# Kernel tuning notes

Measured on AMD Instinct MI355X. Metric: run time of the kernel, lower is better.

## Reference

```python
import jax, jax.numpy as jnp
import numpy as np

EMBED, VOCAB, NUM_DIGEST, EXPAND = 128, 50257, 4, 4


def _mueller_hash(k):
    # https://stackoverflow.com/a/12996028 , uint32 wraparound semantics
    k = (k >> np.uint32(16) ^ k) * np.uint32(73244475)
    k = (k >> np.uint32(16) ^ k) * np.uint32(73244475)
    k = k >> np.uint32(16) ^ k
    return k


def setup_inputs() -> dict:
    key = jax.random.key(0)
    k_tok, k_tab, k_w1, k_w2 = jax.random.split(key, 4)
    # bloom ledger hash indices (exact replication of bloom_ledger)
    ids = np.arange(VOCAB, dtype=np.uint32)
    i_list, j_list = [], []
    for _ in range(NUM_DIGEST):
        ids = _mueller_hash(ids)
        i_list.append(ids % VOCAB)
        ids = _mueller_hash(ids)
        j_list.append(ids % VOCAB)
    bloom_i = jnp.asarray(np.concatenate(i_list).astype(np.int32))
    bloom_j = jnp.asarray(np.concatenate(j_list).astype(np.int32))
    hidden = EMBED * EXPAND
    return {
        "tokens": jax.random.randint(k_tok, (8, 4096), 0, VOCAB, dtype=jnp.int32),
        "table": jax.random.normal(k_tab, (VOCAB, EMBED), jnp.float32) / np.sqrt(EMBED),
        "bloom_i": bloom_i,
        "bloom_j": bloom_j,
        "w1": jax.random.normal(k_w1, (EMBED, hidden), jnp.float32) / np.sqrt(EMBED),
        "b1": jnp.zeros((hidden,), jnp.float32),
        "w2": jax.random.normal(k_w2, (hidden, EMBED), jnp.float32) / np.sqrt(hidden),
        "b2": jnp.zeros((EMBED,), jnp.float32),
    }


def reference(tokens, table, bloom_i, bloom_j, w1, b1, w2, b2):
    vocab = table.shape[0]
    num_digest = bloom_i.shape[0] // vocab
    scale = jnp.asarray(1.0 / np.sqrt(num_digest), table.dtype)
    # bloom @ table as a scatter-add: A[i] += scale * table[j]  -> [vocab, embed]
    agg = jnp.zeros_like(table).at[bloom_i].add(scale * table[bloom_j])
    # one_hot(tokens) @ (bloom @ table) == row gather
    x = agg[tokens]                      # [B, S, embed]
    h = jax.nn.gelu(x @ w1 + b1)         # [B, S, hidden]
    return h @ w2 + b2                   # [B, S, embed]
```

## Files before the change

### kernel.cpp

```cpp
#include <hip/hip_runtime.h>
#include <hip/hip_bf16.h>
#include <stdint.h>

#define EMBED  128
#define HIDDEN 512
#define TB     64
#define CAP    32

typedef __attribute__((ext_vector_type(8))) short short8v;
typedef __attribute__((ext_vector_type(4))) float f32x4;

__device__ __forceinline__ ushort f2bf(float f) {
    uint32_t b = __float_as_uint(f);
    uint32_t r = (b + 0x7FFFu + ((b >> 16) & 1u)) >> 16;
    return (ushort)r;
}

__device__ __forceinline__ float gelu_fast(float x) {
    float x2 = x * x;
    float u  = x * fmaf(0.035677408136f, x2, 0.7978845608f);
    float t  = __expf(2.0f * u);
    return x - x * __frcp_rn(t + 1.0f);
}

__global__ __launch_bounds__(256)
void prep_kernel(const float* __restrict__ w1, const float* __restrict__ w2,
                 ushort* __restrict__ W1t, ushort* __restrict__ W2t,
                 int* __restrict__ cnt, int vocab) {
    __shared__ float T[32][33];
    int b = blockIdx.x;
    int t = threadIdx.x;
    if (b < 128) {
        const float* in; ushort* outp; int inCols, outCols, tr, tc;
        if (b < 64) {
            in = w1; outp = W1t; inCols = 512; outCols = 128;
            tr = b >> 4; tc = b & 15;
        } else {
            int b2 = b - 64;
            in = w2; outp = W2t; inCols = 128; outCols = 512;
            tr = b2 >> 2; tc = b2 & 3;
        }
        int r  = t >> 3;
        int c4 = (t & 7) * 4;
        float4 v = *(const float4*)&in[(size_t)(tr * 32 + r) * inCols + tc * 32 + c4];
        T[c4 + 0][r] = v.x; T[c4 + 1][r] = v.y; T[c4 + 2][r] = v.z; T[c4 + 3][r] = v.w;
        __syncthreads();
        ushort o[4];
        #pragma unroll
        for (int i = 0; i < 4; ++i) o[i] = f2bf(T[r][c4 + i]);
        *(ushort4*)&outp[(size_t)(tc * 32 + r) * outCols + tr * 32 + c4] = *(ushort4*)o;
    } else {
        int i = (b - 128) * 256 + t;
        if (i < vocab) cnt[i] = 0;
    }
}

__global__ __launch_bounds__(256)
void bucket_kernel(const int* __restrict__ bi, const int* __restrict__ bj,
                   int* __restrict__ cnt, int* __restrict__ csr, int nk) {
    int k = blockIdx.x * blockDim.x + threadIdx.x;
    if (k >= nk) return;
    int i = bi[k];
    int slot = atomicAdd(&cnt[i], 1);
    if (slot < CAP) csr[(size_t)i * CAP + slot] = bj[k];
}

__global__ __launch_bounds__(512)
void mlp_mfma_kernel(const int*    __restrict__ tokens,
                     const float*  __restrict__ table,
                     const int*    __restrict__ cnt,
                     const int*    __restrict__ csr,
                     const ushort* __restrict__ W1t,
                     const ushort* __restrict__ W2t,
                     const float*  __restrict__ b1,
                     const float*  __restrict__ b2,
                     float*        __restrict__ out) {
    __shared__ ushort Xs[TB * EMBED];
    __shared__ ushort Hs[TB * HIDDEN];

    const int t    = threadIdx.x;
    const int lane = t & 63;
    const int wv   = t >> 6;
    const int base = blockIdx.x * TB;
    const int l15  = lane & 15;
    const int lhi  = lane >> 4;

    {
        int r    = t >> 3;
        int coff = (t & 7) * 16;
        int tok  = tokens[base + r];
        int m    = min(cnt[tok], CAP);
        const int* jrow = csr + (size_t)tok * CAP;
        f32x4 xa0 = {0.f,0.f,0.f,0.f}, xa1 = {0.f,0.f,0.f,0.f};
        f32x4 xa2 = {0.f,0.f,0.f,0.f}, xa3 = {0.f,0.f,0.f,0.f};
        for (int e = 0; e < m; ++e) {
            int j = jrow[e];
            const float* trp = table + (size_t)j * EMBED + coff;
            float4 v0 = *(const float4*)(trp);
            float4 v1 = *(const float4*)(trp + 4);
            float4 v2 = *(const float4*)(trp + 8);
            float4 v3 = *(const float4*)(trp + 12);
            xa0 += (f32x4){v0.x, v0.y, v0.z, v0.w};
            xa1 += (f32x4){v1.x, v1.y, v1.z, v1.w};
            xa2 += (f32x4){v2.x, v2.y, v2.z, v2.w};
            xa3 += (f32x4){v3.x, v3.y, v3.z, v3.w};
        }
        ushort u[16];
        #pragma unroll
        for (int q = 0; q < 4; ++q) {
            u[q]      = f2bf(0.5f * xa0[q]);
            u[4 + q]  = f2bf(0.5f * xa1[q]);
            u[8 + q]  = f2bf(0.5f * xa2[q]);
            u[12 + q] = f2bf(0.5f * xa3[q]);
        }
        int g0 = (t & 7) * 2;
        #pragma unroll
        for (int h = 0; h < 2; ++h)
            *(short8v*)&Xs[r * EMBED + ((g0 + h) ^ (r & 7)) * 8] = *(short8v*)&u[h * 8];
    }
    __syncthreads();

    f32x4 acc1[4][4];
    #pragma unroll
    for (int n = 0; n < 4; ++n) {
        float bv = b1[wv * 64 + n * 16 + l15];
        #pragma unroll
        for (int m = 0; m < 4; ++m) acc1[m][n] = (f32x4){bv, bv, bv, bv};
    }

    #pragma unroll
    for (int kk = 0; kk < EMBED / 32; ++kk) {
        short8v a[4];
        #pragma unroll
        for (int m = 0; m < 4; ++m) {
            int r = m * 16 + l15;
            int g = (kk * 4 + lhi) ^ (r & 7);
            a[m] = *(const short8v*)&Xs[r * EMBED + g * 8];
        }
        #pragma unroll
        for (int n = 0; n < 4; ++n) {
            int col = wv * 64 + n * 16 + l15;
            short8v b = *(const short8v*)(W1t + (size_t)col * EMBED + kk * 32 + lhi * 8);
            #pragma unroll
            for (int m = 0; m < 4; ++m)
                acc1[m][n] = __builtin_amdgcn_mfma_f32_16x16x32_bf16(a[m], b, acc1[m][n], 0, 0, 0);
        }
    }

    #pragma unroll
    for (int n = 0; n < 4; ++n) {
        int col = wv * 64 + n * 16 + l15;
        #pragma unroll
        for (int m = 0; m < 4; ++m)
            #pragma unroll
            for (int q = 0; q < 4; ++q) {
                int row = m * 16 + lhi * 4 + q;
                float hv = gelu_fast(acc1[m][n][q]);
                int g = (col >> 3) ^ (row & 7);
                Hs[row * HIDDEN + g * 8 + (col & 7)] = f2bf(hv);
            }
    }
    __syncthreads();

    f32x4 acc2[4];
    {
        float bv = b2[wv * 16 + l15];
        #pragma unroll
        for (int m = 0; m < 4; ++m) acc2[m] = (f32x4){bv, bv, bv, bv};
    }
    #pragma unroll
    for (int kk = 0; kk < HIDDEN / 32; ++kk) {
        short8v a[4];
        #pragma unroll
        for (int m = 0; m < 4; ++m) {
            int r = m * 16 + l15;
            int g = (kk * 4 + lhi) ^ (r & 7);
            a[m] = *(const short8v*)&Hs[r * HIDDEN + g * 8];
        }
        int col = wv * 16 + l15;
        short8v b = *(const short8v*)(W2t + (size_t)col * HIDDEN + kk * 32 + lhi * 8);
        #pragma unroll
        for (int m = 0; m < 4; ++m)
            acc2[m] = __builtin_amdgcn_mfma_f32_16x16x32_bf16(a[m], b, acc2[m], 0, 0, 0);
    }

    #pragma unroll
    for (int m = 0; m < 4; ++m)
        #pragma unroll
        for (int q = 0; q < 4; ++q) {
            int row = m * 16 + lhi * 4 + q;
            out[(size_t)(base + row) * EMBED + wv * 16 + l15] = acc2[m][q];
        }
}

extern "C" void kernel_launch(void* const* d_in, const int* in_sizes, int n_in,
                              void* d_out, int out_size, void* d_ws, size_t ws_size,
                              hipStream_t stream) {
    const int*   tokens = (const int*)  d_in[0];
    const float* table  = (const float*)d_in[1];
    const int*   bi     = (const int*)  d_in[2];
    const int*   bj     = (const int*)  d_in[3];
    const float* w1     = (const float*)d_in[4];
    const float* b1     = (const float*)d_in[5];
    const float* w2     = (const float*)d_in[6];
    const float* b2     = (const float*)d_in[7];
    float* out = (float*)d_out;

    const int vocab = in_sizes[1] / EMBED;
    const int nk    = in_sizes[2];
    const int ntok  = in_sizes[0];

    char* ws = (char*)d_ws;
    size_t off = 0;
    auto alloc = [&](size_t b) { size_t o = off; off += (b + 255) & ~(size_t)255; return o; };
    ushort* W1t = (ushort*)(ws + alloc((size_t)EMBED * HIDDEN * 2));
    ushort* W2t = (ushort*)(ws + alloc((size_t)EMBED * HIDDEN * 2));
    int*    csr = (int*)   (ws + alloc((size_t)vocab * CAP * 4));
    int*    cnt = (int*)   (ws + alloc((size_t)vocab * 4));

    int zeroBlocks = (vocab + 255) / 256;
    prep_kernel<<<128 + zeroBlocks, 256, 0, stream>>>(w1, w2, W1t, W2t, cnt, vocab);

    bucket_kernel<<<(nk + 255) / 256, 256, 0, stream>>>(bi, bj, cnt, csr, nk);

    mlp_mfma_kernel<<<ntok / TB, 512, 0, stream>>>(tokens, table, cnt, csr,
                                                   W1t, W2t, b1, b2, out);
}
```

Measured before the change: 68.35 us.

## Split token aggregation gather into a separate wave-per-token kernel

Moves the bloom-row gather and sum out of the MLP kernel into a new kernel where one wave handles one token, with each lane loading a float2 of the row, and writes bf16 aggregated rows to workspace. The MLP kernel then just loads the bf16 rows into LDS. The aim is more memory-level parallelism for the irregular gather, since the fused version only had 512 blocks with 8 threads per token. The cost is an extra launch and a round trip of the intermediate through global memory.

```diff
diff --git a/kernel.cpp b/kernel.cpp
--- a/kernel.cpp
+++ b/kernel.cpp
@@ -65,11 +65,32 @@
     if (slot < CAP) csr[(size_t)i * CAP + slot] = bj[k];
 }
 
+__global__ __launch_bounds__(256)
+void agg_kernel(const int*   __restrict__ tokens,
+                const float* __restrict__ table,
+                const int*   __restrict__ cnt,
+                const int*   __restrict__ csr,
+                ushort*      __restrict__ aggbf, int ntok) {
+    int wid  = (blockIdx.x * blockDim.x + threadIdx.x) >> 6;
+    int lane = threadIdx.x & 63;
+    if (wid >= ntok) return;
+    int tok = tokens[wid];
+    int m = min(cnt[tok], CAP);
+    const int* jrow = csr + (size_t)tok * CAP;
+    float a0 = 0.f, a1 = 0.f;
+    for (int e = 0; e < m; ++e) {
+        int j = jrow[e];
+        float2 v = *(const float2*)&table[(size_t)j * EMBED + lane * 2];
+        a0 += v.x; a1 += v.y;
+    }
+    ushort2 o;
+    o.x = f2bf(0.5f * a0);
+    o.y = f2bf(0.5f * a1);
+    *(ushort2*)&aggbf[(size_t)wid * EMBED + lane * 2] = o;
+}
+
 __global__ __launch_bounds__(512)
-void mlp_mfma_kernel(const int*    __restrict__ tokens,
-                     const float*  __restrict__ table,
-                     const int*    __restrict__ cnt,
-                     const int*    __restrict__ csr,
+void mlp_mfma_kernel(const ushort* __restrict__ aggbf,
                      const ushort* __restrict__ W1t,
                      const ushort* __restrict__ W2t,
                      const float*  __restrict__ b1,
@@ -86,37 +107,15 @@
     const int lhi  = lane >> 4;
 
     {
-        int r    = t >> 3;
-        int coff = (t & 7) * 16;
-        int tok  = tokens[base + r];
-        int m    = min(cnt[tok], CAP);
-        const int* jrow = csr + (size_t)tok * CAP;
-        f32x4 xa0 = {0.f,0.f,0.f,0.f}, xa1 = {0.f,0.f,0.f,0.f};
-        f32x4 xa2 = {0.f,0.f,0.f,0.f}, xa3 = {0.f,0.f,0.f,0.f};
-        for (int e = 0; e < m; ++e) {
-            int j = jrow[e];
-            const float* trp = table + (size_t)j * EMBED + coff;
-            float4 v0 = *(const float4*)(trp);
-            float4 v1 = *(const float4*)(trp + 4);
-            float4 v2 = *(const float4*)(trp + 8);
-            float4 v3 = *(const float4*)(trp + 12);
-            xa0 += (f32x4){v0.x, v0.y, v0.z, v0.w};
-            xa1 += (f32x4){v1.x, v1.y, v1.z, v1.w};
-            xa2 += (f32x4){v2.x, v2.y, v2.z, v2.w};
-            xa3 += (f32x4){v3.x, v3.y, v3.z, v3.w};
-        }
-        ushort u[16];
-        #pragma unroll
-        for (int q = 0; q < 4; ++q) {
-            u[q]      = f2bf(0.5f * xa0[q]);
-            u[4 + q]  = f2bf(0.5f * xa1[q]);
-            u[8 + q]  = f2bf(0.5f * xa2[q]);
-            u[12 + q] = f2bf(0.5f * xa3[q]);
-        }
+        int r  = t >> 3;
         int g0 = (t & 7) * 2;
-        #pragma unroll
-        for (int h = 0; h < 2; ++h)
-            *(short8v*)&Xs[r * EMBED + ((g0 + h) ^ (r & 7)) * 8] = *(short8v*)&u[h * 8];
+        const ushort* src = aggbf + (size_t)(base + r) * EMBED;
+        #pragma unroll
+        for (int h = 0; h < 2; ++h) {
+            int g = g0 + h;
+            short8v v = *(const short8v*)(src + g * 8);
+            *(short8v*)&Xs[r * EMBED + (g ^ (r & 7)) * 8] = v;
+        }
     }
     __syncthreads();
 
@@ -213,16 +212,18 @@
     char* ws = (char*)d_ws;
     size_t off = 0;
     auto alloc = [&](size_t b) { size_t o = off; off += (b + 255) & ~(size_t)255; return o; };
-    ushort* W1t = (ushort*)(ws + alloc((size_t)EMBED * HIDDEN * 2));
-    ushort* W2t = (ushort*)(ws + alloc((size_t)EMBED * HIDDEN * 2));
-    int*    csr = (int*)   (ws + alloc((size_t)vocab * CAP * 4));
-    int*    cnt = (int*)   (ws + alloc((size_t)vocab * 4));
+    ushort* W1t   = (ushort*)(ws + alloc((size_t)EMBED * HIDDEN * 2));
+    ushort* W2t   = (ushort*)(ws + alloc((size_t)EMBED * HIDDEN * 2));
+    ushort* aggbf = (ushort*)(ws + alloc((size_t)ntok * EMBED * 2));
+    int*    csr   = (int*)   (ws + alloc((size_t)vocab * CAP * 4));
+    int*    cnt   = (int*)   (ws + alloc((size_t)vocab * 4));
 
     int zeroBlocks = (vocab + 255) / 256;
     prep_kernel<<<128 + zeroBlocks, 256, 0, stream>>>(w1, w2, W1t, W2t, cnt, vocab);
 
     bucket_kernel<<<(nk + 255) / 256, 256, 0, stream>>>(bi, bj, cnt, csr, nk);
 
-    mlp_mfma_kernel<<<ntok / TB, 512, 0, stream>>>(tokens, table, cnt, csr,
-                                                   W1t, W2t, b1, b2, out);
-}
+    agg_kernel<<<(ntok * 64) / 256, 256, 0, stream>>>(tokens, table, cnt, csr, aggbf, ntok);
+
+    mlp_mfma_kernel<<<ntok / TB, 512, 0, stream>>>(aggbf, W1t, W2t, b1, b2, out);
+}
```

Result: slower. 74.33 us (+8.8%).

## Split hidden dimension into two halves to shrink LDS and registers; prefetch gather rows

Applied to the files above, without the earlier changes.

Processes the hidden layer in two 256-wide halves, computing GEMM1+GELU into a half-sized shared buffer and accumulating GEMM2 per half, which halves the H tile in LDS and the acc1 register footprint so more blocks can reside per CU. Also restructures the embedding gather into a fixed 8-iteration, unroll-2 loop with predicated loads (reading row 0 for absent entries) to raise memory-level parallelism. The cost is an extra pair of barriers per half and some wasted loads for tokens with fewer than 8 bloom entries.

```diff
diff --git a/kernel.cpp b/kernel.cpp
--- a/kernel.cpp
+++ b/kernel.cpp
@@ -5,6 +5,7 @@
 #define EMBED  128
 #define HIDDEN 512
 #define TB     64
+#define HHALF  256
 #define CAP    32
 
 typedef __attribute__((ext_vector_type(8))) short short8v;
@@ -76,7 +77,7 @@
                      const float*  __restrict__ b2,
                      float*        __restrict__ out) {
     __shared__ ushort Xs[TB * EMBED];
-    __shared__ ushort Hs[TB * HIDDEN];
+    __shared__ ushort Hs[TB * HHALF];
 
     const int t    = threadIdx.x;
     const int lane = t & 63;
@@ -93,7 +94,22 @@
         const int* jrow = csr + (size_t)tok * CAP;
         f32x4 xa0 = {0.f,0.f,0.f,0.f}, xa1 = {0.f,0.f,0.f,0.f};
         f32x4 xa2 = {0.f,0.f,0.f,0.f}, xa3 = {0.f,0.f,0.f,0.f};
-        for (int e = 0; e < m; ++e) {
+        #pragma unroll 2
+        for (int e = 0; e < 8; ++e) {
+            int j = (e < m) ? jrow[e] : 0;
+            const float* trp = table + (size_t)j * EMBED + coff;
+            float4 v0 = *(const float4*)(trp);
+            float4 v1 = *(const float4*)(trp + 4);
+            float4 v2 = *(const float4*)(trp + 8);
+            float4 v3 = *(const float4*)(trp + 12);
+            if (e < m) {
+                xa0 += (f32x4){v0.x, v0.y, v0.z, v0.w};
+                xa1 += (f32x4){v1.x, v1.y, v1.z, v1.w};
+                xa2 += (f32x4){v2.x, v2.y, v2.z, v2.w};
+                xa3 += (f32x4){v3.x, v3.y, v3.z, v3.w};
+            }
+        }
+        for (int e = 8; e < m; ++e) {
             int j = jrow[e];
             const float* trp = table + (size_t)j * EMBED + coff;
             float4 v0 = *(const float4*)(trp);
@@ -120,68 +136,72 @@
     }
     __syncthreads();
 
-    f32x4 acc1[4][4];
-    #pragma unroll
-    for (int n = 0; n < 4; ++n) {
-        float bv = b1[wv * 64 + n * 16 + l15];
-        #pragma unroll
-        for (int m = 0; m < 4; ++m) acc1[m][n] = (f32x4){bv, bv, bv, bv};
-    }
-
-    #pragma unroll
-    for (int kk = 0; kk < EMBED / 32; ++kk) {
-        short8v a[4];
-        #pragma unroll
-        for (int m = 0; m < 4; ++m) {
-            int r = m * 16 + l15;
-            int g = (kk * 4 + lhi) ^ (r & 7);
-            a[m] = *(const short8v*)&Xs[r * EMBED + g * 8];
-        }
-        #pragma unroll
-        for (int n = 0; n < 4; ++n) {
-            int col = wv * 64 + n * 16 + l15;
-            short8v b = *(const short8v*)(W1t + (size_t)col * EMBED + kk * 32 + lhi * 8);
-            #pragma unroll
-            for (int m = 0; m < 4; ++m)
-                acc1[m][n] = __builtin_amdgcn_mfma_f32_16x16x32_bf16(a[m], b, acc1[m][n], 0, 0, 0);
-        }
-    }
-
-    #pragma unroll
-    for (int n = 0; n < 4; ++n) {
-        int col = wv * 64 + n * 16 + l15;
-        #pragma unroll
-        for (int m = 0; m < 4; ++m)
-            #pragma unroll
-            for (int q = 0; q < 4; ++q) {
-                int row = m * 16 + lhi * 4 + q;
-                float hv = gelu_fast(acc1[m][n][q]);
-                int g = (col >> 3) ^ (row & 7);
-                Hs[row * HIDDEN + g * 8 + (col & 7)] = f2bf(hv);
-            }
-    }
-    __syncthreads();
-
     f32x4 acc2[4];
     {
         float bv = b2[wv * 16 + l15];
         #pragma unroll
         for (int m = 0; m < 4; ++m) acc2[m] = (f32x4){bv, bv, bv, bv};
     }
+
     #pragma unroll
-    for (int kk = 0; kk < HIDDEN / 32; ++kk) {
-        short8v a[4];
-        #pragma unroll
-        for (int m = 0; m < 4; ++m) {
-            int r = m * 16 + l15;
-            int g = (kk * 4 + lhi) ^ (r & 7);
-            a[m] = *(const short8v*)&Hs[r * HIDDEN + g * 8];
-        }
-        int col = wv * 16 + l15;
-        short8v b = *(const short8v*)(W2t + (size_t)col * HIDDEN + kk * 32 + lhi * 8);
-        #pragma unroll
-        for (int m = 0; m < 4; ++m)
-            acc2[m] = __builtin_amdgcn_mfma_f32_16x16x32_bf16(a[m], b, acc2[m], 0, 0, 0);
+    for (int h = 0; h < 2; ++h) {
+        f32x4 acc1[4][2];
+        #pragma unroll
+        for (int n = 0; n < 2; ++n) {
+            float bv = b1[h * HHALF + wv * 32 + n * 16 + l15];
+            #pragma unroll
+            for (int m = 0; m < 4; ++m) acc1[m][n] = (f32x4){bv, bv, bv, bv};
+        }
+        #pragma unroll
+        for (int kk = 0; kk < EMBED / 32; ++kk) {
+            short8v a[4];
+            #pragma unroll
+            for (int m = 0; m < 4; ++m) {
+                int r = m * 16 + l15;
+                int g = (kk * 4 + lhi) ^ (r & 7);
+                a[m] = *(const short8v*)&Xs[r * EMBED + g * 8];
+            }
+            #pragma unroll
+            for (int n = 0; n < 2; ++n) {
+                int col = h * HHALF + wv * 32 + n * 16 + l15;
+                short8v b = *(const short8v*)(W1t + (size_t)col * EMBED + kk * 32 + lhi * 8);
+                #pragma unroll
+                for (int m = 0; m < 4; ++m)
+                    acc1[m][n] = __builtin_amdgcn_mfma_f32_16x16x32_bf16(a[m], b, acc1[m][n], 0, 0, 0);
+            }
+        }
+
+        #pragma unroll
+        for (int n = 0; n < 2; ++n) {
+            int colh = wv * 32 + n * 16 + l15;
+            #pragma unroll
+            for (int m = 0; m < 4; ++m)
+                #pragma unroll
+                for (int q = 0; q < 4; ++q) {
+                    int row = m * 16 + lhi * 4 + q;
+                    float hv = gelu_fast(acc1[m][n][q]);
+                    int g = (colh >> 3) ^ (row & 7);
+                    Hs[row * HHALF + g * 8 + (colh & 7)] = f2bf(hv);
+                }
+        }
+        __syncthreads();
+
+        #pragma unroll
+        for (int kk = 0; kk < HHALF / 32; ++kk) {
+            short8v a[4];
+            #pragma unroll
+            for (int m = 0; m < 4; ++m) {
+                int r = m * 16 + l15;
+                int g = (kk * 4 + lhi) ^ (r & 7);
+                a[m] = *(const short8v*)&Hs[r * HHALF + g * 8];
+            }
+            int col = wv * 16 + l15;
+            short8v b = *(const short8v*)(W2t + (size_t)col * HIDDEN + h * HHALF + kk * 32 + lhi * 8);
+            #pragma unroll
+            for (int m = 0; m < 4; ++m)
+                acc2[m] = __builtin_amdgcn_mfma_f32_16x16x32_bf16(a[m], b, acc2[m], 0, 0, 0);
+        }
+        __syncthreads();
     }
 
     #pragma unroll
```

Result: faster. 57.76 us (-15.5%).
